# Optimization experiments

Measured on AMD Instinct MI355X. Metric: run time of the kernel, lower is better.

The kernel has to match this reference:

```python
import jax, jax.numpy as jnp
import numpy as np

N = 384
NEG = jnp.float32(-1e30)


def setup_inputs() -> dict:
    key = jax.random.key(0)
    k1, k2, k3 = jax.random.split(key, 3)
    od = jax.random.uniform(k1, (N, N), dtype=jnp.float32) * 100.0  # OD demand (nn.Parameter in torch)
    adj = jax.random.randint(k2, (N, N), 0, 2, dtype=jnp.int32)     # binary adjacency
    dist = jax.random.uniform(k3, (N, N), dtype=jnp.float32) * 10.0 + 1.0  # free-flow times t0
    return {"od": od, "adj": adj, "dist": dist, "lambda_param": 1, "capacity": 500}


def _logit_assignment(od, adj, dist, lam):
    # Vectorized equivalent of the torch nested-loop logit assignment.
    # Paths have cutoff=2 edges: direct (o->d) and two-hop (o->k->d, k!=o, k!=d).
    n = od.shape[0]
    eye = jnp.eye(n, dtype=bool)
    # demand gated by od>0; diagonal OD pairs contribute no edge flow
    demand = jnp.where((od > 0) & ~eye, od, 0.0)
    A = (adj > 0) & ~eye  # usable directed edges (self-loops never on a simple path)
    # direct-path logits [o,d]
    l1 = jnp.where(A, -lam * dist, NEG)
    # two-hop path mask/times [o,k,d]; simple path => k!=o (in A), k!=d (in A), o!=d
    hop = A[:, :, None] & A[None, :, :] & (~eye)[:, None, :]
    t2 = dist[:, :, None] + dist[None, :, :]
    l2 = jnp.where(hop, -lam * t2, NEG)
    # stable softmax over {direct} u {all k} per OD pair
    m = jnp.maximum(l1, l2.max(axis=1))  # [o,d]
    e1 = jnp.where(A, jnp.exp(l1 - m), 0.0)
    e2 = jnp.where(hop, jnp.exp(l2 - m[:, None, :]), 0.0)
    Z = e1 + e2.sum(axis=1)  # [o,d]
    safe = Z > 0
    w = jnp.where(safe, demand / jnp.where(safe, Z, 1.0), 0.0)  # demand * (1/Z)
    # scatter assigned flow onto edges
    flows = w * e1                                       # direct edge (o,d)
    flows = flows + jnp.einsum('od,okd->ok', w, e2)      # first hop edge (o,k)
    flows = flows + jnp.einsum('od,okd->kd', w, e2)      # second hop edge (k,d)
    return flows


def reference(od, adj, dist, lambda_param, capacity):
    # max_iter=1 in the source, and the post-assignment BPR travel-time update is
    # under no_grad and only mutates G after the single assignment, so the returned
    # flow_results equals one logit assignment on the free-flow distances.
    lam = jnp.float32(lambda_param)
    return _logit_assignment(od, adj, dist, lam)
```

## Files before the change

### kernel.cpp

```cpp
#include <hip/hip_runtime.h>
#include <math.h>

#define NN 384
#define NT 24
#define NTILES (NT * NT)

typedef __attribute__((ext_vector_type(8))) short short8;
typedef __attribute__((ext_vector_type(4))) float v4f;

__device__ __forceinline__ unsigned short f2bf(float f) {
    union { float f; unsigned u; } v; v.f = f;
    unsigned r = (v.u + 0x7FFFu + ((v.u >> 16) & 1u)) >> 16;
    return (unsigned short)r;
}
__device__ __forceinline__ float bf2f(unsigned short h) {
    union { unsigned u; float f; } v; v.u = ((unsigned)h) << 16;
    return v.f;
}

__global__ void build_p_kernel(const int* __restrict__ adj,
                               const float* __restrict__ dist,
                               const int* __restrict__ lam_ptr,
                               unsigned short* __restrict__ P16,
                               unsigned short* __restrict__ PT16) {
    int idx = blockIdx.x * 256 + threadIdx.x;
    int i = idx / NN;
    int j = idx - i * NN;
    float lam = (float)(*lam_ptr);
    float p = (adj[idx] > 0 && i != j) ? expf(-lam * dist[idx]) : 0.0f;
    unsigned short h = f2bf(p);
    P16[idx] = h;
    PT16[j * NN + i] = h;
}

__global__ __launch_bounds__(64) void v_kernel(const unsigned short* __restrict__ P16,
                                               const unsigned short* __restrict__ PT16,
                                               const float* __restrict__ od,
                                               float* __restrict__ V32,
                                               unsigned short* __restrict__ V16,
                                               unsigned short* __restrict__ VT16) {
    int t = blockIdx.x;
    int i0 = (t / NT) * 16, j0 = (t % NT) * 16;
    int lane = threadIdx.x;
    int col = lane & 15, quad = lane >> 4;
    v4f acc = {0.f, 0.f, 0.f, 0.f};
    const short8* arow = (const short8*)(P16 + (i0 + col) * NN + quad * 8);
    const short8* brow = (const short8*)(PT16 + (j0 + col) * NN + quad * 8);
#pragma unroll
    for (int k0 = 0; k0 < NN / 32; ++k0) {
        short8 a = arow[k0 * 4];
        short8 b = brow[k0 * 4];
        acc = __builtin_amdgcn_mfma_f32_16x16x32_bf16(a, b, acc, 0, 0, 0);
    }
#pragma unroll
    for (int r = 0; r < 4; ++r) {
        int i = i0 + quad * 4 + r, j = j0 + col;
        int idx = i * NN + j;
        float denom = bf2f(P16[idx]) + acc[r];
        float o = od[idx];
        float v = (i != j && o > 0.0f && denom > 0.0f) ? o / denom : 0.0f;
        V32[idx] = v;
        unsigned short h = f2bf(v);
        V16[idx] = h;
        VT16[j * NN + i] = h;
    }
}

__global__ __launch_bounds__(64) void flows_kernel(const unsigned short* __restrict__ P16,
                                                   const unsigned short* __restrict__ PT16,
                                                   const unsigned short* __restrict__ V16,
                                                   const unsigned short* __restrict__ VT16,
                                                   const float* __restrict__ V32,
                                                   const int* __restrict__ adj,
                                                   const float* __restrict__ dist,
                                                   const int* __restrict__ lam_ptr,
                                                   float* __restrict__ out) {
    int t = blockIdx.x;
    int i0 = (t / NT) * 16, j0 = (t % NT) * 16;
    int lane = threadIdx.x;
    int col = lane & 15, quad = lane >> 4;
    v4f accW = {0.f, 0.f, 0.f, 0.f};
    v4f accU = {0.f, 0.f, 0.f, 0.f};
    const short8* aW = (const short8*)(V16 + (i0 + col) * NN + quad * 8);
    const short8* bW = (const short8*)(P16 + (j0 + col) * NN + quad * 8);
    const short8* aU = (const short8*)(PT16 + (i0 + col) * NN + quad * 8);
    const short8* bU = (const short8*)(VT16 + (j0 + col) * NN + quad * 8);
#pragma unroll
    for (int k0 = 0; k0 < NN / 32; ++k0) {
        short8 a0 = aW[k0 * 4];
        short8 b0 = bW[k0 * 4];
        short8 a1 = aU[k0 * 4];
        short8 b1 = bU[k0 * 4];
        accW = __builtin_amdgcn_mfma_f32_16x16x32_bf16(a0, b0, accW, 0, 0, 0);
        accU = __builtin_amdgcn_mfma_f32_16x16x32_bf16(a1, b1, accU, 0, 0, 0);
    }
    float lam = (float)(*lam_ptr);
#pragma unroll
    for (int r = 0; r < 4; ++r) {
        int i = i0 + quad * 4 + r, j = j0 + col;
        int idx = i * NN + j;
        float p = (adj[idx] > 0 && i != j) ? expf(-lam * dist[idx]) : 0.0f;
        out[idx] = p * (V32[idx] + accW[r] + accU[r]);
    }
}

extern "C" void kernel_launch(void* const* d_in, const int* in_sizes, int n_in,
                              void* d_out, int out_size, void* d_ws, size_t ws_size,
                              hipStream_t stream) {
    const float* od   = (const float*)d_in[0];
    const int*   adj  = (const int*)d_in[1];
    const float* dist = (const float*)d_in[2];
    const int*   lam  = (const int*)d_in[3];
    float* out = (float*)d_out;

    unsigned short* P16  = (unsigned short*)d_ws;
    unsigned short* PT16 = P16 + NN * NN;
    unsigned short* V16  = PT16 + NN * NN;
    unsigned short* VT16 = V16 + NN * NN;
    float*          V32  = (float*)(VT16 + NN * NN);

    build_p_kernel<<<NTILES, 256, 0, stream>>>(adj, dist, lam, P16, PT16);
    v_kernel<<<NTILES, 64, 0, stream>>>(P16, PT16, od, V32, V16, VT16);
    flows_kernel<<<NTILES, 64, 0, stream>>>(P16, PT16, V16, VT16, V32, adj, dist, lam, out);
}
```

Baseline: 75.15 us.

## Fuse three kernels into one cooperative kernel with grid-wide syncs

Replaces the three separate launches (build P, compute V, compute flows) with a single cooperative kernel of 576 single-wave blocks that uses grid.sync() between phases. The P-build phase now has each thread handle four contiguous elements with vectorized loads and stores. The aim is to remove launch overhead and inter-kernel gaps. The cost is the latency of the grid barriers, and the launch requires all 576 blocks to be co-resident.

```diff
diff --git a/kernel.cpp b/kernel.cpp
--- a/kernel.cpp
+++ b/kernel.cpp
@@ -1,5 +1,8 @@
 #include <hip/hip_runtime.h>
+#include <hip/hip_cooperative_groups.h>
 #include <math.h>
+
+namespace cg = cooperative_groups;
 
 #define NN 384
 #define NT 24
@@ -7,100 +10,102 @@
 
 typedef __attribute__((ext_vector_type(8))) short short8;
 typedef __attribute__((ext_vector_type(4))) float v4f;
+typedef __attribute__((ext_vector_type(4))) unsigned short ushort4v;
 
 __device__ __forceinline__ unsigned short f2bf(float f) {
     union { float f; unsigned u; } v; v.f = f;
-    unsigned r = (v.u + 0x7FFFu + ((v.u >> 16) & 1u)) >> 16;
-    return (unsigned short)r;
+    return (unsigned short)((v.u + 0x7FFFu + ((v.u >> 16) & 1u)) >> 16);
 }
 __device__ __forceinline__ float bf2f(unsigned short h) {
     union { unsigned u; float f; } v; v.u = ((unsigned)h) << 16;
     return v.f;
 }
 
-__global__ void build_p_kernel(const int* __restrict__ adj,
-                               const float* __restrict__ dist,
-                               const int* __restrict__ lam_ptr,
-                               unsigned short* __restrict__ P16,
-                               unsigned short* __restrict__ PT16) {
-    int idx = blockIdx.x * 256 + threadIdx.x;
-    int i = idx / NN;
-    int j = idx - i * NN;
-    float lam = (float)(*lam_ptr);
-    float p = (adj[idx] > 0 && i != j) ? expf(-lam * dist[idx]) : 0.0f;
-    unsigned short h = f2bf(p);
-    P16[idx] = h;
-    PT16[j * NN + i] = h;
-}
+__global__ __launch_bounds__(64) void fused_kernel(
+    const float* __restrict__ od, const int* __restrict__ adj,
+    const float* __restrict__ dist, const int* __restrict__ lam_ptr,
+    float* __restrict__ out,
+    unsigned short* __restrict__ P16, unsigned short* __restrict__ PT16,
+    unsigned short* __restrict__ V16, unsigned short* __restrict__ VT16,
+    float* __restrict__ V32)
+{
+    cg::grid_group grid = cg::this_grid();
+    const int lane = threadIdx.x;
+    const int blk = blockIdx.x;
+    const float lam = (float)(*lam_ptr);
+    const int i0 = (blk / NT) * 16, j0 = (blk % NT) * 16;
+    const int col = lane & 15, quad = lane >> 4;
 
-__global__ __launch_bounds__(64) void v_kernel(const unsigned short* __restrict__ P16,
-                                               const unsigned short* __restrict__ PT16,
-                                               const float* __restrict__ od,
-                                               float* __restrict__ V32,
-                                               unsigned short* __restrict__ V16,
-                                               unsigned short* __restrict__ VT16) {
-    int t = blockIdx.x;
-    int i0 = (t / NT) * 16, j0 = (t % NT) * 16;
-    int lane = threadIdx.x;
-    int col = lane & 15, quad = lane >> 4;
-    v4f acc = {0.f, 0.f, 0.f, 0.f};
-    const short8* arow = (const short8*)(P16 + (i0 + col) * NN + quad * 8);
-    const short8* brow = (const short8*)(PT16 + (j0 + col) * NN + quad * 8);
+    {
+        int base = (blk * 64 + lane) * 4;
+        int i = base / NN;
+        int j = base - i * NN;
+        float4 d4 = *(const float4*)(dist + base);
+        int4   a4 = *(const int4*)(adj + base);
+        float dv[4] = {d4.x, d4.y, d4.z, d4.w};
+        int   av[4] = {a4.x, a4.y, a4.z, a4.w};
+        ushort4v h;
 #pragma unroll
-    for (int k0 = 0; k0 < NN / 32; ++k0) {
-        short8 a = arow[k0 * 4];
-        short8 b = brow[k0 * 4];
-        acc = __builtin_amdgcn_mfma_f32_16x16x32_bf16(a, b, acc, 0, 0, 0);
+        for (int e = 0; e < 4; ++e) {
+            float p = (av[e] > 0 && i != (j + e)) ? expf(-lam * dv[e]) : 0.0f;
+            unsigned short hb = f2bf(p);
+            h[e] = hb;
+            PT16[(j + e) * NN + i] = hb;
+        }
+        *(ushort4v*)(P16 + base) = h;
     }
+
+    grid.sync();
+
+    {
+        v4f acc = {0.f, 0.f, 0.f, 0.f};
+        const short8* arow = (const short8*)(P16 + (i0 + col) * NN + quad * 8);
+        const short8* brow = (const short8*)(PT16 + (j0 + col) * NN + quad * 8);
 #pragma unroll
-    for (int r = 0; r < 4; ++r) {
-        int i = i0 + quad * 4 + r, j = j0 + col;
-        int idx = i * NN + j;
-        float denom = bf2f(P16[idx]) + acc[r];
-        float o = od[idx];
-        float v = (i != j && o > 0.0f && denom > 0.0f) ? o / denom : 0.0f;
-        V32[idx] = v;
-        unsigned short h = f2bf(v);
-        V16[idx] = h;
-        VT16[j * NN + i] = h;
+        for (int k0 = 0; k0 < NN / 32; ++k0) {
+            short8 a = arow[k0 * 4];
+            short8 b = brow[k0 * 4];
+            acc = __builtin_amdgcn_mfma_f32_16x16x32_bf16(a, b, acc, 0, 0, 0);
+        }
+#pragma unroll
+        for (int r = 0; r < 4; ++r) {
+            int i = i0 + quad * 4 + r, j = j0 + col;
+            int idx = i * NN + j;
+            float denom = bf2f(P16[idx]) + acc[r];
+            float o = od[idx];
+            float v = (i != j && o > 0.0f && denom > 0.0f) ? o / denom : 0.0f;
+            V32[idx] = v;
+            unsigned short hb = f2bf(v);
+            V16[idx] = hb;
+            VT16[j * NN + i] = hb;
+        }
     }
-}
 
-__global__ __launch_bounds__(64) void flows_kernel(const unsigned short* __restrict__ P16,
-                                                   const unsigned short* __restrict__ PT16,
-                                                   const unsigned short* __restrict__ V16,
-                                                   const unsigned short* __restrict__ VT16,
-                                                   const float* __restrict__ V32,
-                                                   const int* __restrict__ adj,
-                                                   const float* __restrict__ dist,
-                                                   const int* __restrict__ lam_ptr,
-                                                   float* __restrict__ out) {
-    int t = blockIdx.x;
-    int i0 = (t / NT) * 16, j0 = (t % NT) * 16;
-    int lane = threadIdx.x;
-    int col = lane & 15, quad = lane >> 4;
-    v4f accW = {0.f, 0.f, 0.f, 0.f};
-    v4f accU = {0.f, 0.f, 0.f, 0.f};
-    const short8* aW = (const short8*)(V16 + (i0 + col) * NN + quad * 8);
-    const short8* bW = (const short8*)(P16 + (j0 + col) * NN + quad * 8);
-    const short8* aU = (const short8*)(PT16 + (i0 + col) * NN + quad * 8);
-    const short8* bU = (const short8*)(VT16 + (j0 + col) * NN + quad * 8);
+    grid.sync();
+
+    {
+        v4f accW = {0.f, 0.f, 0.f, 0.f};
+        v4f accU = {0.f, 0.f, 0.f, 0.f};
+        const short8* aW = (const short8*)(V16 + (i0 + col) * NN + quad * 8);
+        const short8* bW = (const short8*)(P16 + (j0 + col) * NN + quad * 8);
+        const short8* aU = (const short8*)(PT16 + (i0 + col) * NN + quad * 8);
+        const short8* bU = (const short8*)(VT16 + (j0 + col) * NN + quad * 8);
 #pragma unroll
-    for (int k0 = 0; k0 < NN / 32; ++k0) {
-        short8 a0 = aW[k0 * 4];
-        short8 b0 = bW[k0 * 4];
-        short8 a1 = aU[k0 * 4];
-        short8 b1 = bU[k0 * 4];
-        accW = __builtin_amdgcn_mfma_f32_16x16x32_bf16(a0, b0, accW, 0, 0, 0);
-        accU = __builtin_amdgcn_mfma_f32_16x16x32_bf16(a1, b1, accU, 0, 0, 0);
-    }
-    float lam = (float)(*lam_ptr);
+        for (int k0 = 0; k0 < NN / 32; ++k0) {
+            short8 a0 = aW[k0 * 4];
+            short8 b0 = bW[k0 * 4];
+            short8 a1 = aU[k0 * 4];
+            short8 b1 = bU[k0 * 4];
+            accW = __builtin_amdgcn_mfma_f32_16x16x32_bf16(a0, b0, accW, 0, 0, 0);
+            accU = __builtin_amdgcn_mfma_f32_16x16x32_bf16(a1, b1, accU, 0, 0, 0);
+        }
 #pragma unroll
-    for (int r = 0; r < 4; ++r) {
-        int i = i0 + quad * 4 + r, j = j0 + col;
-        int idx = i * NN + j;
-        float p = (adj[idx] > 0 && i != j) ? expf(-lam * dist[idx]) : 0.0f;
-        out[idx] = p * (V32[idx] + accW[r] + accU[r]);
+        for (int r = 0; r < 4; ++r) {
+            int i = i0 + quad * 4 + r, j = j0 + col;
+            int idx = i * NN + j;
+            float p = (adj[idx] > 0 && i != j) ? expf(-lam * dist[idx]) : 0.0f;
+            out[idx] = p * (V32[idx] + accW[r] + accU[r]);
+        }
     }
 }
 
@@ -119,7 +124,9 @@
     unsigned short* VT16 = V16 + NN * NN;
     float*          V32  = (float*)(VT16 + NN * NN);
 
-    build_p_kernel<<<NTILES, 256, 0, stream>>>(adj, dist, lam, P16, PT16);
-    v_kernel<<<NTILES, 64, 0, stream>>>(P16, PT16, od, V32, V16, VT16);
-    flows_kernel<<<NTILES, 64, 0, stream>>>(P16, PT16, V16, VT16, V32, adj, dist, lam, out);
+    void* args[] = {(void*)&od, (void*)&adj, (void*)&dist, (void*)&lam,
+                    (void*)&out, (void*)&P16, (void*)&PT16, (void*)&V16,
+                    (void*)&VT16, (void*)&V32};
+    hipLaunchCooperativeKernel((const void*)fused_kernel, dim3(NTILES), dim3(64),
+                               args, 0, stream);
 }
```

Result: slower. 213.9 us (+184.6%).

## Fuse V and flows kernels by recomputing V row/column strips per tile

Applied to the files above, without the earlier changes.

Merges the V computation and flow GEMMs into one kernel: each 16x16 output tile recomputes the full row strip and column strip of V it needs, using 4 waves, keeps them in LDS, then wave 0 does the final two MFMA reductions. This removes one kernel launch and the global round-trip of V in fp32/bf16 and its transpose. In exchange, it recomputes V redundantly (roughly 48x more GEMM work for V) and leaves three waves idle in the final phase. It also swaps the division for a fast reciprocal.

```diff
diff --git a/kernel.cpp b/kernel.cpp
--- a/kernel.cpp
+++ b/kernel.cpp
@@ -4,14 +4,15 @@
 #define NN 384
 #define NT 24
 #define NTILES (NT * NT)
+#define LDSW 392
 
 typedef __attribute__((ext_vector_type(8))) short short8;
 typedef __attribute__((ext_vector_type(4))) float v4f;
+typedef __attribute__((ext_vector_type(4))) unsigned short ushort4v;
 
 __device__ __forceinline__ unsigned short f2bf(float f) {
     union { float f; unsigned u; } v; v.f = f;
-    unsigned r = (v.u + 0x7FFFu + ((v.u >> 16) & 1u)) >> 16;
-    return (unsigned short)r;
+    return (unsigned short)((v.u + 0x7FFFu + ((v.u >> 16) & 1u)) >> 16);
 }
 __device__ __forceinline__ float bf2f(unsigned short h) {
     union { unsigned u; float f; } v; v.u = ((unsigned)h) << 16;
@@ -33,74 +34,95 @@
     PT16[j * NN + i] = h;
 }
 
-__global__ __launch_bounds__(64) void v_kernel(const unsigned short* __restrict__ P16,
-                                               const unsigned short* __restrict__ PT16,
-                                               const float* __restrict__ od,
-                                               float* __restrict__ V32,
-                                               unsigned short* __restrict__ V16,
-                                               unsigned short* __restrict__ VT16) {
-    int t = blockIdx.x;
-    int i0 = (t / NT) * 16, j0 = (t % NT) * 16;
-    int lane = threadIdx.x;
-    int col = lane & 15, quad = lane >> 4;
-    v4f acc = {0.f, 0.f, 0.f, 0.f};
-    const short8* arow = (const short8*)(P16 + (i0 + col) * NN + quad * 8);
-    const short8* brow = (const short8*)(PT16 + (j0 + col) * NN + quad * 8);
+__global__ __launch_bounds__(256) void fused_tile_kernel(
+    const unsigned short* __restrict__ P16,
+    const unsigned short* __restrict__ PT16,
+    const float* __restrict__ od,
+    const int* __restrict__ adj,
+    const float* __restrict__ dist,
+    const int* __restrict__ lam_ptr,
+    float* __restrict__ out)
+{
+    __shared__ __align__(16) unsigned short Vr[16][LDSW];
+    __shared__ __align__(16) unsigned short VcT[16][LDSW];
+    __shared__ float Vd[16][17];
+
+    const int t = blockIdx.x;
+    const int it = t / NT, jt = t % NT;
+    const int i0 = it * 16, j0 = jt * 16;
+    const int tid = threadIdx.x;
+    const int wave = tid >> 6;
+    const int lane = tid & 63;
+    const int col = lane & 15, quad = lane >> 4;
+
+    short8 a1[12], b2[12];
 #pragma unroll
-    for (int k0 = 0; k0 < NN / 32; ++k0) {
-        short8 a = arow[k0 * 4];
-        short8 b = brow[k0 * 4];
-        acc = __builtin_amdgcn_mfma_f32_16x16x32_bf16(a, b, acc, 0, 0, 0);
+    for (int k0 = 0; k0 < 12; ++k0) {
+        a1[k0] = *(const short8*)(P16 + (i0 + col) * NN + k0 * 32 + quad * 8);
+        b2[k0] = *(const short8*)(PT16 + (j0 + col) * NN + k0 * 32 + quad * 8);
     }
+
+    for (int n0 = wave * 6; n0 < wave * 6 + 6; ++n0) {
+        v4f acc = {0.f, 0.f, 0.f, 0.f};
 #pragma unroll
-    for (int r = 0; r < 4; ++r) {
-        int i = i0 + quad * 4 + r, j = j0 + col;
-        int idx = i * NN + j;
-        float denom = bf2f(P16[idx]) + acc[r];
-        float o = od[idx];
-        float v = (i != j && o > 0.0f && denom > 0.0f) ? o / denom : 0.0f;
-        V32[idx] = v;
-        unsigned short h = f2bf(v);
-        V16[idx] = h;
-        VT16[j * NN + i] = h;
+        for (int k0 = 0; k0 < 12; ++k0) {
+            short8 b = *(const short8*)(PT16 + (n0 * 16 + col) * NN + k0 * 32 + quad * 8);
+            acc = __builtin_amdgcn_mfma_f32_16x16x32_bf16(a1[k0], b, acc, 0, 0, 0);
+        }
+#pragma unroll
+        for (int r = 0; r < 4; ++r) {
+            int i = i0 + quad * 4 + r, j = n0 * 16 + col;
+            int idx = i * NN + j;
+            float denom = bf2f(P16[idx]) + acc[r];
+            float o = od[idx];
+            float v = (i != j && o > 0.f && denom > 0.f)
+                          ? o * __builtin_amdgcn_rcpf(denom) : 0.f;
+            Vr[quad * 4 + r][j] = f2bf(v);
+            if (n0 == jt) Vd[quad * 4 + r][col] = v;
+        }
     }
-}
 
-__global__ __launch_bounds__(64) void flows_kernel(const unsigned short* __restrict__ P16,
-                                                   const unsigned short* __restrict__ PT16,
-                                                   const unsigned short* __restrict__ V16,
-                                                   const unsigned short* __restrict__ VT16,
-                                                   const float* __restrict__ V32,
-                                                   const int* __restrict__ adj,
-                                                   const float* __restrict__ dist,
-                                                   const int* __restrict__ lam_ptr,
-                                                   float* __restrict__ out) {
-    int t = blockIdx.x;
-    int i0 = (t / NT) * 16, j0 = (t % NT) * 16;
-    int lane = threadIdx.x;
-    int col = lane & 15, quad = lane >> 4;
-    v4f accW = {0.f, 0.f, 0.f, 0.f};
-    v4f accU = {0.f, 0.f, 0.f, 0.f};
-    const short8* aW = (const short8*)(V16 + (i0 + col) * NN + quad * 8);
-    const short8* bW = (const short8*)(P16 + (j0 + col) * NN + quad * 8);
-    const short8* aU = (const short8*)(PT16 + (i0 + col) * NN + quad * 8);
-    const short8* bU = (const short8*)(VT16 + (j0 + col) * NN + quad * 8);
+    for (int m0 = wave * 6; m0 < wave * 6 + 6; ++m0) {
+        v4f acc = {0.f, 0.f, 0.f, 0.f};
 #pragma unroll
-    for (int k0 = 0; k0 < NN / 32; ++k0) {
-        short8 a0 = aW[k0 * 4];
-        short8 b0 = bW[k0 * 4];
-        short8 a1 = aU[k0 * 4];
-        short8 b1 = bU[k0 * 4];
-        accW = __builtin_amdgcn_mfma_f32_16x16x32_bf16(a0, b0, accW, 0, 0, 0);
-        accU = __builtin_amdgcn_mfma_f32_16x16x32_bf16(a1, b1, accU, 0, 0, 0);
+        for (int k0 = 0; k0 < 12; ++k0) {
+            short8 a = *(const short8*)(P16 + (m0 * 16 + col) * NN + k0 * 32 + quad * 8);
+            acc = __builtin_amdgcn_mfma_f32_16x16x32_bf16(a, b2[k0], acc, 0, 0, 0);
+        }
+#pragma unroll
+        for (int r = 0; r < 4; ++r) {
+            int i = m0 * 16 + quad * 4 + r, j = j0 + col;
+            int idx = i * NN + j;
+            float denom = bf2f(P16[idx]) + acc[r];
+            float o = od[idx];
+            float v = (i != j && o > 0.f && denom > 0.f)
+                          ? o * __builtin_amdgcn_rcpf(denom) : 0.f;
+            VcT[col][i] = f2bf(v);
+        }
     }
-    float lam = (float)(*lam_ptr);
+
+    __syncthreads();
+
+    if (wave == 0) {
+        v4f accW = {0.f, 0.f, 0.f, 0.f};
+        v4f accU = {0.f, 0.f, 0.f, 0.f};
 #pragma unroll
-    for (int r = 0; r < 4; ++r) {
-        int i = i0 + quad * 4 + r, j = j0 + col;
-        int idx = i * NN + j;
-        float p = (adj[idx] > 0 && i != j) ? expf(-lam * dist[idx]) : 0.0f;
-        out[idx] = p * (V32[idx] + accW[r] + accU[r]);
+        for (int k0 = 0; k0 < 12; ++k0) {
+            short8 aW = *(const short8*)(&Vr[col][k0 * 32 + quad * 8]);
+            short8 bW = *(const short8*)(P16 + (j0 + col) * NN + k0 * 32 + quad * 8);
+            accW = __builtin_amdgcn_mfma_f32_16x16x32_bf16(aW, bW, accW, 0, 0, 0);
+            short8 aU = *(const short8*)(PT16 + (i0 + col) * NN + k0 * 32 + quad * 8);
+            short8 bU = *(const short8*)(&VcT[col][k0 * 32 + quad * 8]);
+            accU = __builtin_amdgcn_mfma_f32_16x16x32_bf16(aU, bU, accU, 0, 0, 0);
+        }
+        float lam = (float)(*lam_ptr);
+#pragma unroll
+        for (int r = 0; r < 4; ++r) {
+            int i = i0 + quad * 4 + r, j = j0 + col;
+            int idx = i * NN + j;
+            float p = (adj[idx] > 0 && i != j) ? expf(-lam * dist[idx]) : 0.f;
+            out[idx] = p * (Vd[quad * 4 + r][col] + accW[r] + accU[r]);
+        }
     }
 }
 
@@ -115,11 +137,7 @@
 
     unsigned short* P16  = (unsigned short*)d_ws;
     unsigned short* PT16 = P16 + NN * NN;
-    unsigned short* V16  = PT16 + NN * NN;
-    unsigned short* VT16 = V16 + NN * NN;
-    float*          V32  = (float*)(VT16 + NN * NN);
 
     build_p_kernel<<<NTILES, 256, 0, stream>>>(adj, dist, lam, P16, PT16);
-    v_kernel<<<NTILES, 64, 0, stream>>>(P16, PT16, od, V32, V16, VT16);
-    flows_kernel<<<NTILES, 64, 0, stream>>>(P16, PT16, V16, VT16, V32, adj, dist, lam, out);
+    fused_tile_kernel<<<NTILES, 256, 0, stream>>>(P16, PT16, od, adj, dist, lam, out);
 }
```

After: 126.5 us. 1.68x slower.
